# Performance work log

Measured on AMD Instinct MI355X. Metric: run time of the kernel, lower is better.

Reference implementation:

```python
import jax, jax.numpy as jnp
import numpy as np

N = 50000      # nodes
E = 800000     # edges
D = 128        # feature dim
L = 3          # gcn layers
EPS = 1e-5     # batchnorm eps


def setup_inputs() -> dict:
    key = jax.random.key(0)
    ks = jax.random.split(key, 6)
    s = (2.0 / (D + D)) ** 0.5  # xavier-uniform scale proxy
    x = jax.random.normal(ks[0], (N, D), jnp.float32)
    edge_index = jax.random.randint(ks[1], (2, E), 0, N, dtype=jnp.int32)
    conv_w = jax.random.normal(ks[2], (L, D, D), jnp.float32) * s
    conv_b = jnp.zeros((L, D), jnp.float32)
    bn_gamma = jnp.ones((2, D), jnp.float32)
    bn_beta = jnp.zeros((2, D), jnp.float32)
    mlp_w = jax.random.normal(ks[3], (2, D, D), jnp.float32) * s
    mlp_b = jnp.zeros((2, D), jnp.float32)
    out_w = jax.random.normal(ks[4], (D, 1), jnp.float32) * s
    out_b = jnp.zeros((1,), jnp.float32)
    return dict(x=x, edge_index=edge_index, conv_w=conv_w, conv_b=conv_b,
                bn_gamma=bn_gamma, bn_beta=bn_beta, mlp_w=mlp_w, mlp_b=mlp_b,
                out_w=out_w, out_b=out_b)


def _batchnorm(h, gamma, beta):
    # train-mode BN: batch stats over nodes (biased variance, as torch uses for normalization)
    mean = jnp.mean(h, axis=0)
    var = jnp.mean((h - mean) ** 2, axis=0)
    return (h - mean) * jax.lax.rsqrt(var + EPS) * gamma + beta


def reference(x, conv_w, conv_b, bn_gamma, bn_beta, mlp_w, mlp_b, out_w, out_b, edge_index):
    # --- GCN normalization (PyG GCNConv default: add self-loops, sym norm) ---
    loops = jnp.arange(N, dtype=edge_index.dtype)
    src = jnp.concatenate([edge_index[0], loops])  # [E+N]
    dst = jnp.concatenate([edge_index[1], loops])
    deg = jax.ops.segment_sum(jnp.ones_like(dst, jnp.float32), dst, num_segments=N)
    dis = jnp.where(deg > 0, jax.lax.rsqrt(jnp.maximum(deg, 1.0)), 0.0)  # deg^-1/2
    norm = (dis[src] * dis[dst])[:, None]  # [E+N, 1]

    def gcn_conv(h, W, b):
        h = h @ W                                     # [N, D] transform
        msg = h[src] * norm                           # gather + scale, [E+N, D]
        return jax.ops.segment_sum(msg, dst, num_segments=N) + b

    # dropout is identity (training=False)
    h = x
    # layers 0..L-2: conv -> bn -> relu
    for layer in range(L - 1):
        h = gcn_conv(h, conv_w[layer], conv_b[layer])
        h = _batchnorm(h, bn_gamma[layer], bn_beta[layer])
        h = jax.nn.relu(h)
    # last conv: relu(conv), then bns[-1] applied AGAIN (faithful to original quirk)
    h = jax.nn.relu(gcn_conv(h, conv_w[L - 1], conv_b[L - 1]))
    h = _batchnorm(h, bn_gamma[-1], bn_beta[-1])

    # --- MLP classifier head: relu hidden layers, sigmoid output ---
    for i in range(mlp_w.shape[0]):
        h = jax.nn.relu(h @ mlp_w[i] + mlp_b[i])
    out = jax.nn.sigmoid(h @ out_w + out_b)  # [N, 1]
    return out
```

## Files before the change

kernel.cpp:

```cpp
#include <hip/hip_runtime.h>
#include <hip/hip_bf16.h>

#define NN 50000
#define EE 800000
#define DD 128
#define OVCAP 8192

typedef __attribute__((ext_vector_type(8))) short short8;
typedef __attribute__((ext_vector_type(4))) float floatx4;

__device__ __forceinline__ unsigned short f2bf(float f) {
    unsigned int x = __float_as_uint(f);
    unsigned int r = x + 0x7fffu + ((x >> 16) & 1u);
    return (unsigned short)(r >> 16);
}
__device__ __forceinline__ float2 bf2x2(unsigned int u) {
    return make_float2(__uint_as_float(u << 16), __uint_as_float(u & 0xffff0000u));
}

__global__ void k_wprep(const float* __restrict__ conv_w, const float* __restrict__ mlp_w,
                        unsigned short* __restrict__ Wf, unsigned int* __restrict__ hsrow,
                        int* __restrict__ cnt, float* __restrict__ stats,
                        int* __restrict__ ovcnt, int* __restrict__ ell) {
    int g = blockIdx.x * 256 + threadIdx.x;
    if (g < 81920) {
        int m = g >> 14;
        int idx = g & 16383;
        int j  = idx & 7;
        int n  = (idx >> 3) & 15;
        int q  = (idx >> 7) & 3;
        int kk = (idx >> 9) & 3;
        int nt = (idx >> 11) & 1;
        int w  = (idx >> 12) & 3;
        int k = kk * 32 + q * 8 + j;
        int c = w * 32 + nt * 16 + n;
        const float* src = (m < 3) ? (conv_w + m * 16384) : (mlp_w + (m - 3) * 16384);
        Wf[g] = f2bf(src[k * 128 + c]);
    } else if (g < 81984) {
        hsrow[g - 81920] = 0u;
    } else if (g < 133184) {
        cnt[g - 81984] = 0;
    } else if (g < 133952) {
        stats[g - 133184] = 0.f;
    } else if (g < 133968) {
        ovcnt[g - 133952] = 0;
    } else if (g < 533968) {
        ((int4*)ell)[g - 133968] = make_int4(NN, NN, NN, NN);
    }
}

__global__ void k_fill(const int* __restrict__ ei, int* __restrict__ cnt,
                       int* __restrict__ ell, int* __restrict__ ovcnt,
                       int2* __restrict__ ov) {
    const int team = blockIdx.x & 7;
    const int lo = team * 6250, hi = lo + 6250;
    const int tIdx = (blockIdx.x >> 3) * 256 + threadIdx.x;
    for (int e = tIdx; e < EE; e += 65536) {
        int d = ei[EE + e];
        if (d >= lo && d < hi) {
            int s = ei[e];
            if ((unsigned)s < (unsigned)NN) {
                int slot = atomicAdd(&cnt[d], 1);
                if (slot < 32) {
                    ell[d * 32 + slot] = s;
                } else {
                    int op = atomicAdd(ovcnt, 1);
                    if (op < OVCAP) ov[op] = make_int2(d, s);
                }
            }
        }
    }
}

#define LSTR 136
template<int PRO>
__global__ __launch_bounds__(256) void k_gemm_conv(const void* __restrict__ INv,
                                                   const unsigned short* __restrict__ Wf,
                                                   const int* __restrict__ cnt,
                                                   const float* __restrict__ cs,
                                                   const float* __restrict__ css,
                                                   const float* __restrict__ gamma,
                                                   const float* __restrict__ beta,
                                                   unsigned short* __restrict__ OUT) {
    __shared__ unsigned short Al[32 * LSTR];
    __shared__ float bnscL[128], bnshL[128];
    const int tid = threadIdx.x;
    const int lane = tid & 63;
    const int w = tid >> 6;
    const int row0 = blockIdx.x * 32;

    if (PRO) {
        if (tid < 128) {
            const float invn = 1.f / (float)NN;
            float mean = cs[tid] * invn;
            float var = css[tid] * invn - mean * mean;
            float sc = gamma[tid] * rsqrtf(fmaxf(var, 0.f) + 1e-5f);
            bnscL[tid] = sc;
            bnshL[tid] = beta[tid] - mean * sc;
        }
        __syncthreads();
    }

    short8 bf[2][4];
    {
        const uint4* Wq = (const uint4*)Wf;
#pragma unroll
        for (int nt = 0; nt < 2; ++nt)
#pragma unroll
            for (int kk = 0; kk < 4; ++kk) {
                uint4 u = Wq[((w * 2 + nt) * 4 + kk) * 64 + lane];
                bf[nt][kk] = *(short8*)&u;
            }
    }

    {
        int r = tid >> 3, ko8 = (tid & 7) * 16;
        int gr = row0 + r;
        unsigned short tmp[16];
        if (PRO == 0) {
            const float* IN = (const float*)INv;
#pragma unroll
            for (int i = 0; i < 4; ++i) {
                float4 v = make_float4(0.f, 0.f, 0.f, 0.f);
                if (gr < NN) v = *(const float4*)&IN[(size_t)gr * DD + ko8 + i * 4];
                tmp[i * 4 + 0] = f2bf(v.x); tmp[i * 4 + 1] = f2bf(v.y);
                tmp[i * 4 + 2] = f2bf(v.z); tmp[i * 4 + 3] = f2bf(v.w);
            }
        } else {
            const unsigned int* inu = (const unsigned int*)INv;
#pragma unroll
            for (int i = 0; i < 2; ++i) {
                uint4 u = make_uint4(0u, 0u, 0u, 0u);
                if (gr < NN) u = *(const uint4*)&inu[(size_t)gr * 64 + (ko8 >> 1) + i * 4];
                float2 p0 = bf2x2(u.x), p1 = bf2x2(u.y), p2 = bf2x2(u.z), p3 = bf2x2(u.w);
                float vv[8] = {p0.x, p0.y, p1.x, p1.y, p2.x, p2.y, p3.x, p3.y};
#pragma unroll
                for (int j = 0; j < 8; ++j) {
                    float t2 = fmaf(vv[j], bnscL[ko8 + i * 8 + j], bnshL[ko8 + i * 8 + j]);
                    tmp[i * 8 + j] = f2bf(fmaxf(t2, 0.f));
                }
            }
        }
#pragma unroll
        for (int j = 0; j < 2; ++j)
            *(uint4*)&Al[r * LSTR + ko8 + j * 8] = ((uint4*)tmp)[j];
    }
    __syncthreads();

    const int n = lane & 15, q = lane >> 4;
    floatx4 acc[2][2];
#pragma unroll
    for (int mt = 0; mt < 2; ++mt)
#pragma unroll
        for (int nt = 0; nt < 2; ++nt)
            acc[mt][nt] = (floatx4){0.f, 0.f, 0.f, 0.f};

#pragma unroll
    for (int kk = 0; kk < 4; ++kk) {
        int ko = kk * 32 + q * 8;
#pragma unroll
        for (int mt = 0; mt < 2; ++mt) {
            short8 a = *(const short8*)&Al[(mt * 16 + n) * LSTR + ko];
            acc[mt][0] = __builtin_amdgcn_mfma_f32_16x16x32_bf16(a, bf[0][kk], acc[mt][0], 0, 0, 0);
            acc[mt][1] = __builtin_amdgcn_mfma_f32_16x16x32_bf16(a, bf[1][kk], acc[mt][1], 0, 0, 0);
        }
    }

#pragma unroll
    for (int mt = 0; mt < 2; ++mt) {
#pragma unroll
        for (int reg = 0; reg < 4; ++reg) {
            int r = row0 + mt * 16 + q * 4 + reg;
            if (r < NN) {
                float sc = rsqrtf((float)cnt[r] + 1.0f);
                OUT[(size_t)r * DD + w * 32 + n]      = f2bf(acc[mt][0][reg] * sc);
                OUT[(size_t)r * DD + w * 32 + 16 + n] = f2bf(acc[mt][1][reg] * sc);
            }
        }
    }
}

__global__ __launch_bounds__(256) void k_mlp_head(const unsigned int* __restrict__ INu,
                                                  const unsigned short* __restrict__ Wf4,
                                                  const unsigned short* __restrict__ Wf5,
                                                  const float* __restrict__ b4,
                                                  const float* __restrict__ b5,
                                                  const float* __restrict__ cs,
                                                  const float* __restrict__ css,
                                                  const float* __restrict__ gamma,
                                                  const float* __restrict__ beta,
                                                  const float* __restrict__ ow,
                                                  const float* __restrict__ ob,
                                                  float* __restrict__ out) {
    __shared__ unsigned short Al[32 * LSTR];
    __shared__ float bnscL[128], bnshL[128];
    __shared__ float redH[4][32];
    const int tid = threadIdx.x;
    const int lane = tid & 63;
    const int w = tid >> 6;
    const int row0 = blockIdx.x * 32;
    const int n = lane & 15, q = lane >> 4;

    if (tid < 128) {
        const float invn = 1.f / (float)NN;
        float mean = cs[tid] * invn;
        float var = css[tid] * invn - mean * mean;
        float sc = gamma[tid] * rsqrtf(fmaxf(var, 0.f) + 1e-5f);
        bnscL[tid] = sc;
        bnshL[tid] = beta[tid] - mean * sc;
    }
    __syncthreads();

    {
        int r = tid >> 3, ko8 = (tid & 7) * 16;
        int gr = row0 + r;
        unsigned short tmp[16];
#pragma unroll
        for (int i = 0; i < 2; ++i) {
            uint4 u = make_uint4(0u, 0u, 0u, 0u);
            if (gr < NN) u = *(const uint4*)&INu[(size_t)gr * 64 + (ko8 >> 1) + i * 4];
            float2 p0 = bf2x2(u.x), p1 = bf2x2(u.y), p2 = bf2x2(u.z), p3 = bf2x2(u.w);
            float vv[8] = {p0.x, p0.y, p1.x, p1.y, p2.x, p2.y, p3.x, p3.y};
#pragma unroll
            for (int j = 0; j < 8; ++j) {
                float t2 = fmaf(vv[j], bnscL[ko8 + i * 8 + j], bnshL[ko8 + i * 8 + j]);
                tmp[i * 8 + j] = f2bf(t2);
            }
        }
#pragma unroll
        for (int j = 0; j < 2; ++j)
            *(uint4*)&Al[r * LSTR + ko8 + j * 8] = ((uint4*)tmp)[j];
    }
    __syncthreads();

    floatx4 acc[2][2];
#pragma unroll
    for (int mt = 0; mt < 2; ++mt)
#pragma unroll
        for (int nt = 0; nt < 2; ++nt)
            acc[mt][nt] = (floatx4){0.f, 0.f, 0.f, 0.f};
    {
        const uint4* Wq = (const uint4*)Wf4;
#pragma unroll
        for (int kk = 0; kk < 4; ++kk) {
            uint4 u0 = Wq[((w * 2 + 0) * 4 + kk) * 64 + lane];
            uint4 u1 = Wq[((w * 2 + 1) * 4 + kk) * 64 + lane];
            int ko = kk * 32 + q * 8;
#pragma unroll
            for (int mt = 0; mt < 2; ++mt) {
                short8 a = *(const short8*)&Al[(mt * 16 + n) * LSTR + ko];
                acc[mt][0] = __builtin_amdgcn_mfma_f32_16x16x32_bf16(a, *(short8*)&u0, acc[mt][0], 0, 0, 0);
                acc[mt][1] = __builtin_amdgcn_mfma_f32_16x16x32_bf16(a, *(short8*)&u1, acc[mt][1], 0, 0, 0);
            }
        }
    }
    __syncthreads();

    {
        float b0c = b4[w * 32 + n], b1c = b4[w * 32 + 16 + n];
#pragma unroll
        for (int mt = 0; mt < 2; ++mt) {
#pragma unroll
            for (int reg = 0; reg < 4; ++reg) {
                int r = mt * 16 + q * 4 + reg;
                Al[r * LSTR + w * 32 + n]      = f2bf(fmaxf(acc[mt][0][reg] + b0c, 0.f));
                Al[r * LSTR + w * 32 + 16 + n] = f2bf(fmaxf(acc[mt][1][reg] + b1c, 0.f));
            }
        }
    }
    __syncthreads();

#pragma unroll
    for (int mt = 0; mt < 2; ++mt)
#pragma unroll
        for (int nt = 0; nt < 2; ++nt)
            acc[mt][nt] = (floatx4){0.f, 0.f, 0.f, 0.f};
    {
        const uint4* Wq = (const uint4*)Wf5;
#pragma unroll
        for (int kk = 0; kk < 4; ++kk) {
            uint4 u0 = Wq[((w * 2 + 0) * 4 + kk) * 64 + lane];
            uint4 u1 = Wq[((w * 2 + 1) * 4 + kk) * 64 + lane];
            int ko = kk * 32 + q * 8;
#pragma unroll
            for (int mt = 0; mt < 2; ++mt) {
                short8 a = *(const short8*)&Al[(mt * 16 + n) * LSTR + ko];
                acc[mt][0] = __builtin_amdgcn_mfma_f32_16x16x32_bf16(a, *(short8*)&u0, acc[mt][0], 0, 0, 0);
                acc[mt][1] = __builtin_amdgcn_mfma_f32_16x16x32_bf16(a, *(short8*)&u1, acc[mt][1], 0, 0, 0);
            }
        }
    }
    {
        float b0c = b5[w * 32 + n], b1c = b5[w * 32 + 16 + n];
        float w0c = ow[w * 32 + n], w1c = ow[w * 32 + 16 + n];
#pragma unroll
        for (int mt = 0; mt < 2; ++mt) {
#pragma unroll
            for (int reg = 0; reg < 4; ++reg) {
                float h0 = fmaxf(acc[mt][0][reg] + b0c, 0.f);
                float h1 = fmaxf(acc[mt][1][reg] + b1c, 0.f);
                float p = fmaf(h0, w0c, h1 * w1c);
                p += __shfl_xor(p, 1);
                p += __shfl_xor(p, 2);
                p += __shfl_xor(p, 4);
                p += __shfl_xor(p, 8);
                if (n == 0) redH[w][mt * 16 + q * 4 + reg] = p;
            }
        }
        __syncthreads();
        if (tid < 32) {
            int r = row0 + tid;
            if (r < NN) {
                float z = (redH[0][tid] + redH[1][tid]) + (redH[2][tid] + redH[3][tid]) + ob[0];
                out[r] = 1.f / (1.f + expf(-z));
            }
        }
    }
}
#undef LSTR

template<int RELU>
__global__ __launch_bounds__(256) void k_gather(const int* __restrict__ cnt,
                                                const int* __restrict__ ell,
                                                const int2* __restrict__ ov,
                                                const int* __restrict__ ovcnt,
                                                const uint4* __restrict__ HSq,
                                                const float* __restrict__ bias,
                                                unsigned short* __restrict__ OUT,
                                                float* __restrict__ colsum,
                                                float* __restrict__ colsumsq) {
    const int tid = threadIdx.x;
    const int lane = tid & 63;
    const int wid = tid >> 6;
    const int c = lane & 15;
    const int jj = lane >> 4;
    const int gwave = blockIdx.x * 4 + wid;
    const int oc = min(*ovcnt, OVCAP);

    float4 bia0 = ((const float4*)bias)[2 * c];
    float4 bia1 = ((const float4*)bias)[2 * c + 1];
    float sum[8], sq[8];
#pragma unroll
    for (int t = 0; t < 8; ++t) { sum[t] = 0.f; sq[t] = 0.f; }

    const uint4 z4 = make_uint4(0u, 0u, 0u, 0u);
    const int4 iz = make_int4(NN, NN, NN, NN);

    int r = gwave;
    int d = 0;
    int4 ia = iz, ib = iz;
    if (r < NN) {
        d = cnt[r];
        const int4* e4 = (const int4*)(ell + (size_t)r * 32);
        ia = e4[jj];
        ib = e4[jj + 4];
    }

    while (r < NN) {
        uint4 s0 = z4;
        if (jj == 0) s0 = HSq[(size_t)r * 16 + c];
        const bool pa = (ia.x != NN), pb = (ib.x != NN);
        uint4 va[4] = {z4, z4, z4, z4}, vb[4] = {z4, z4, z4, z4};
        if (pa) {
            va[0] = HSq[(size_t)ia.x * 16 + c];
            va[1] = HSq[(size_t)ia.y * 16 + c];
            va[2] = HSq[(size_t)ia.z * 16 + c];
            va[3] = HSq[(size_t)ia.w * 16 + c];
        }
        if (pb) {
            vb[0] = HSq[(size_t)ib.x * 16 + c];
            vb[1] = HSq[(size_t)ib.y * 16 + c];
            vb[2] = HSq[(size_t)ib.z * 16 + c];
            vb[3] = HSq[(size_t)ib.w * 16 + c];
        }

        const int rcur = r, dcur = d;

        r += 8192;
        if (r < NN) {
            d = cnt[r];
            const int4* e4 = (const int4*)(ell + (size_t)r * 32);
            ia = e4[jj];
            ib = e4[jj + 4];
        } else {
            ia = iz; ib = iz;
        }

        float a[8];
#pragma unroll
        for (int t = 0; t < 8; ++t) a[t] = 0.f;
        if (jj == 0) {
            float2 p0 = bf2x2(s0.x), p1 = bf2x2(s0.y), p2 = bf2x2(s0.z), p3 = bf2x2(s0.w);
            a[0] += p0.x; a[1] += p0.y; a[2] += p1.x; a[3] += p1.y;
            a[4] += p2.x; a[5] += p2.y; a[6] += p3.x; a[7] += p3.y;
        }
        if (pa) {
#pragma unroll
            for (int t = 0; t < 4; ++t) {
                float2 p0 = bf2x2(va[t].x), p1 = bf2x2(va[t].y);
                float2 p2 = bf2x2(va[t].z), p3 = bf2x2(va[t].w);
                a[0] += p0.x; a[1] += p0.y; a[2] += p1.x; a[3] += p1.y;
                a[4] += p2.x; a[5] += p2.y; a[6] += p3.x; a[7] += p3.y;
            }
        }
        if (pb) {
#pragma unroll
            for (int t = 0; t < 4; ++t) {
                float2 p0 = bf2x2(vb[t].x), p1 = bf2x2(vb[t].y);
                float2 p2 = bf2x2(vb[t].z), p3 = bf2x2(vb[t].w);
                a[0] += p0.x; a[1] += p0.y; a[2] += p1.x; a[3] += p1.y;
                a[4] += p2.x; a[5] += p2.y; a[6] += p3.x; a[7] += p3.y;
            }
        }
        if (dcur > 32) {
            for (int t = 0; t < oc; ++t) {
                int2 e = ov[t];
                if (jj == 0 && e.x == rcur) {
                    uint4 v = HSq[(size_t)e.y * 16 + c];
                    float2 p0 = bf2x2(v.x), p1 = bf2x2(v.y), p2 = bf2x2(v.z), p3 = bf2x2(v.w);
                    a[0] += p0.x; a[1] += p0.y; a[2] += p1.x; a[3] += p1.y;
                    a[4] += p2.x; a[5] += p2.y; a[6] += p3.x; a[7] += p3.y;
                }
            }
        }

#pragma unroll
        for (int t = 0; t < 8; ++t) {
            a[t] += __shfl_xor(a[t], 16);
            a[t] += __shfl_xor(a[t], 32);
        }

        if (jj == 0) {
            float dr = rsqrtf((float)dcur + 1.0f);
            float v[8];
            v[0] = fmaf(dr, a[0], bia0.x); v[1] = fmaf(dr, a[1], bia0.y);
            v[2] = fmaf(dr, a[2], bia0.z); v[3] = fmaf(dr, a[3], bia0.w);
            v[4] = fmaf(dr, a[4], bia1.x); v[5] = fmaf(dr, a[5], bia1.y);
            v[6] = fmaf(dr, a[6], bia1.z); v[7] = fmaf(dr, a[7], bia1.w);
            if (RELU) {
#pragma unroll
                for (int t = 0; t < 8; ++t) v[t] = fmaxf(v[t], 0.f);
            }
            unsigned int p[4];
#pragma unroll
            for (int t = 0; t < 4; ++t)
                p[t] = (unsigned int)f2bf(v[2 * t]) | ((unsigned int)f2bf(v[2 * t + 1]) << 16);
            *(uint4*)&OUT[(size_t)rcur * DD + c * 8] = make_uint4(p[0], p[1], p[2], p[3]);
#pragma unroll
            for (int t = 0; t < 8; ++t) { sum[t] += v[t]; sq[t] += v[t] * v[t]; }
        }
    }

    __shared__ float redS[4][16][8];
    __shared__ float redQ[4][16][8];
    if (jj == 0) {
#pragma unroll
        for (int t = 0; t < 8; ++t) { redS[wid][c][t] = sum[t]; redQ[wid][c][t] = sq[t]; }
    }
    __syncthreads();
    if (tid < 128) {
        int ci = tid >> 3, ct = tid & 7;
        float S = (redS[0][ci][ct] + redS[1][ci][ct]) + (redS[2][ci][ct] + redS[3][ci][ct]);
        float Q = (redQ[0][ci][ct] + redQ[1][ci][ct]) + (redQ[2][ci][ct] + redQ[3][ci][ct]);
        atomicAdd(&colsum[tid], S);
        atomicAdd(&colsumsq[tid], Q);
    }
}

extern "C" void kernel_launch(void* const* d_in, const int* in_sizes, int n_in,
                              void* d_out, int out_size, void* d_ws, size_t ws_size,
                              hipStream_t stream) {
    const float* x      = (const float*)d_in[0];
    const int*   ei     = (const int*)d_in[1];
    const float* conv_w = (const float*)d_in[2];
    const float* conv_b = (const float*)d_in[3];
    const float* bn_g   = (const float*)d_in[4];
    const float* bn_b   = (const float*)d_in[5];
    const float* mlp_w  = (const float*)d_in[6];
    const float* mlp_b  = (const float*)d_in[7];
    const float* out_w  = (const float*)d_in[8];
    const float* out_b  = (const float*)d_in[9];
    float* out = (float*)d_out;

    const size_t ND4 = (size_t)NN * DD * 4;
    char* ws = (char*)d_ws;
    size_t off = 0;
    unsigned short* B0 = (unsigned short*)(ws + off); off += ND4 / 2;
    unsigned short* B1b = (unsigned short*)(ws + off); off += ND4 / 2 + 256;
    int*   cnt     = (int*)  (ws + off); off += 204800;
    float* cs3     = (float*)(ws + off); off += 3 * 512;
    float* css3    = (float*)(ws + off); off += 3 * 512;
    int*   ovcnt   = (int*)  (ws + off); off += 64;
    int2*  ov      = (int2*) (ws + off); off += OVCAP * 8;
    unsigned short* Wfb = (unsigned short*)(ws + off); off += 5 * 16384 * 2;
    int*   ell     = (int*)  (ws + off); off += (size_t)NN * 32 * 4;

    const int gemm_grid = (NN + 31) / 32;
    const int gather_grid = 2048;

    k_wprep<<<2086, 256, 0, stream>>>(conv_w, mlp_w, Wfb,
        (unsigned int*)(B1b + (size_t)NN * DD), cnt, cs3, ovcnt, ell);

    k_fill<<<2048, 256, 0, stream>>>(ei, cnt, ell, ovcnt, ov);

    k_gemm_conv<0><<<gemm_grid, 256, 0, stream>>>(x, Wfb, cnt,
        nullptr, nullptr, nullptr, nullptr, B1b);
    k_gather<0><<<gather_grid, 256, 0, stream>>>(cnt, ell, ov, ovcnt, (const uint4*)B1b, conv_b, B0, cs3, css3);

    k_gemm_conv<1><<<gemm_grid, 256, 0, stream>>>(B0, Wfb + 16384, cnt,
        cs3, css3, bn_g, bn_b, B1b);
    k_gather<0><<<gather_grid, 256, 0, stream>>>(cnt, ell, ov, ovcnt, (const uint4*)B1b, conv_b + DD, B0, cs3 + 128, css3 + 128);

    k_gemm_conv<1><<<gemm_grid, 256, 0, stream>>>(B0, Wfb + 2 * 16384, cnt,
        cs3 + 128, css3 + 128, bn_g + DD, bn_b + DD, B1b);
    k_gather<1><<<gather_grid, 256, 0, stream>>>(cnt, ell, ov, ovcnt, (const uint4*)B1b, conv_b + 2 * DD, B0, cs3 + 256, css3 + 256);

    k_mlp_head<<<gemm_grid, 256, 0, stream>>>((const unsigned int*)B0, Wfb + 3 * 16384, Wfb + 4 * 16384,
        mlp_b, mlp_b + DD, cs3 + 256, css3 + 256, bn_g + DD, bn_b + DD, out_w, out_b, out);
}
```

Measured before the change: 369.8 us.

## Fuse GCN layers and MLP head into one persistent kernel with grid barriers

Replaces the seven per-stage launches (three GEMMs, three gathers, the MLP head) with a single persistent kernel of 1024 blocks. The blocks loop over row tiles and nodes and separate the stages with a software grid barrier built on global atomics. This removes launch gaps and tail effects between the dependent stages. In exchange, the barrier needs all 1024 blocks to be resident at once, which the launch bound of 4 blocks per CU is meant to ensure, and it depends on bc and bg having been zeroed. The gather stride also changes from 8192 to 4096 waves.

```diff
diff --git a/kernel.cpp b/kernel.cpp
--- a/kernel.cpp
+++ b/kernel.cpp
@@ -5,6 +5,10 @@
 #define EE 800000
 #define DD 128
 #define OVCAP 8192
+#define LSTR 136
+#define NTILE 1563
+#define MGRID 1024
+#define GS 4096
 
 typedef __attribute__((ext_vector_type(8))) short short8;
 typedef __attribute__((ext_vector_type(4))) float floatx4;
@@ -16,6 +20,22 @@
 }
 __device__ __forceinline__ float2 bf2x2(unsigned int u) {
     return make_float2(__uint_as_float(u << 16), __uint_as_float(u & 0xffff0000u));
+}
+
+__device__ __forceinline__ void gsync(int* bc, int* bg) {
+    __syncthreads();
+    if (threadIdx.x == 0) {
+        int g = __hip_atomic_load(bg, __ATOMIC_RELAXED, __HIP_MEMORY_SCOPE_AGENT);
+        int a = __hip_atomic_fetch_add(bc, 1, __ATOMIC_ACQ_REL, __HIP_MEMORY_SCOPE_AGENT);
+        if (a == MGRID - 1) {
+            __hip_atomic_store(bc, 0, __ATOMIC_RELAXED, __HIP_MEMORY_SCOPE_AGENT);
+            __hip_atomic_fetch_add(bg, 1, __ATOMIC_ACQ_REL, __HIP_MEMORY_SCOPE_AGENT);
+        } else {
+            while (__hip_atomic_load(bg, __ATOMIC_ACQUIRE, __HIP_MEMORY_SCOPE_AGENT) == g)
+                __builtin_amdgcn_s_sleep(2);
+        }
+    }
+    __syncthreads();
 }
 
 __global__ void k_wprep(const float* __restrict__ conv_w, const float* __restrict__ mlp_w,
@@ -72,25 +92,265 @@
     }
 }
 
-#define LSTR 136
-template<int PRO>
-__global__ __launch_bounds__(256) void k_gemm_conv(const void* __restrict__ INv,
-                                                   const unsigned short* __restrict__ Wf,
-                                                   const int* __restrict__ cnt,
-                                                   const float* __restrict__ cs,
-                                                   const float* __restrict__ css,
-                                                   const float* __restrict__ gamma,
-                                                   const float* __restrict__ beta,
-                                                   unsigned short* __restrict__ OUT) {
+__global__ __launch_bounds__(256, 4) void k_mega(
+        const float* __restrict__ xin, const int* __restrict__ cnt,
+        const int* __restrict__ ell, const int2* __restrict__ ov,
+        const int* __restrict__ ovcnt, const unsigned short* __restrict__ Wfb,
+        const float* __restrict__ conv_b, const float* __restrict__ bn_g,
+        const float* __restrict__ bn_b, const float* __restrict__ mlp_b,
+        const float* __restrict__ out_w, const float* __restrict__ out_b,
+        unsigned short* __restrict__ B0, unsigned short* __restrict__ B1b,
+        float* __restrict__ cs3, float* __restrict__ css3,
+        float* __restrict__ out, int* __restrict__ bc, int* __restrict__ bg) {
     __shared__ unsigned short Al[32 * LSTR];
     __shared__ float bnscL[128], bnshL[128];
+    __shared__ float redH[4][32];
+    __shared__ float redS[4][16][8];
+    __shared__ float redQ[4][16][8];
+
     const int tid = threadIdx.x;
     const int lane = tid & 63;
     const int w = tid >> 6;
-    const int row0 = blockIdx.x * 32;
-
-    if (PRO) {
+    const int oc = min(*ovcnt, OVCAP);
+    const uint4* HSq = (const uint4*)B1b;
+
+    for (int L = 0; L < 3; ++L) {
+        {
+            const bool pro = (L > 0);
+            if (pro && tid < 128) {
+                const float* cs = cs3 + (L - 1) * 128;
+                const float* css = css3 + (L - 1) * 128;
+                const float* gamma = bn_g + (L - 1) * DD;
+                const float* beta = bn_b + (L - 1) * DD;
+                const float invn = 1.f / (float)NN;
+                float mean = cs[tid] * invn;
+                float var = css[tid] * invn - mean * mean;
+                float sc = gamma[tid] * rsqrtf(fmaxf(var, 0.f) + 1e-5f);
+                bnscL[tid] = sc;
+                bnshL[tid] = beta[tid] - mean * sc;
+            }
+            __syncthreads();
+
+            short8 bf[2][4];
+            {
+                const uint4* Wq = (const uint4*)(Wfb + (size_t)L * 16384);
+#pragma unroll
+                for (int nt = 0; nt < 2; ++nt)
+#pragma unroll
+                    for (int kk = 0; kk < 4; ++kk) {
+                        uint4 u = Wq[((w * 2 + nt) * 4 + kk) * 64 + lane];
+                        bf[nt][kk] = *(short8*)&u;
+                    }
+            }
+            const int n = lane & 15, q = lane >> 4;
+
+            for (int t = blockIdx.x; t < NTILE; t += MGRID) {
+                const int row0 = t * 32;
+                {
+                    int r = tid >> 3, ko8 = (tid & 7) * 16;
+                    int gr = row0 + r;
+                    unsigned short tmp[16];
+                    if (!pro) {
+#pragma unroll
+                        for (int i = 0; i < 4; ++i) {
+                            float4 v = make_float4(0.f, 0.f, 0.f, 0.f);
+                            if (gr < NN) v = *(const float4*)&xin[(size_t)gr * DD + ko8 + i * 4];
+                            tmp[i * 4 + 0] = f2bf(v.x); tmp[i * 4 + 1] = f2bf(v.y);
+                            tmp[i * 4 + 2] = f2bf(v.z); tmp[i * 4 + 3] = f2bf(v.w);
+                        }
+                    } else {
+                        const unsigned int* inu = (const unsigned int*)B0;
+#pragma unroll
+                        for (int i = 0; i < 2; ++i) {
+                            uint4 u = make_uint4(0u, 0u, 0u, 0u);
+                            if (gr < NN) u = *(const uint4*)&inu[(size_t)gr * 64 + (ko8 >> 1) + i * 4];
+                            float2 p0 = bf2x2(u.x), p1 = bf2x2(u.y), p2 = bf2x2(u.z), p3 = bf2x2(u.w);
+                            float vv[8] = {p0.x, p0.y, p1.x, p1.y, p2.x, p2.y, p3.x, p3.y};
+#pragma unroll
+                            for (int j = 0; j < 8; ++j) {
+                                float t2 = fmaf(vv[j], bnscL[ko8 + i * 8 + j], bnshL[ko8 + i * 8 + j]);
+                                tmp[i * 8 + j] = f2bf(fmaxf(t2, 0.f));
+                            }
+                        }
+                    }
+#pragma unroll
+                    for (int j = 0; j < 2; ++j)
+                        *(uint4*)&Al[r * LSTR + ko8 + j * 8] = ((uint4*)tmp)[j];
+                }
+                __syncthreads();
+
+                floatx4 acc[2][2];
+#pragma unroll
+                for (int mt = 0; mt < 2; ++mt)
+#pragma unroll
+                    for (int nt = 0; nt < 2; ++nt)
+                        acc[mt][nt] = (floatx4){0.f, 0.f, 0.f, 0.f};
+#pragma unroll
+                for (int kk = 0; kk < 4; ++kk) {
+                    int ko = kk * 32 + q * 8;
+#pragma unroll
+                    for (int mt = 0; mt < 2; ++mt) {
+                        short8 a = *(const short8*)&Al[(mt * 16 + n) * LSTR + ko];
+                        acc[mt][0] = __builtin_amdgcn_mfma_f32_16x16x32_bf16(a, bf[0][kk], acc[mt][0], 0, 0, 0);
+                        acc[mt][1] = __builtin_amdgcn_mfma_f32_16x16x32_bf16(a, bf[1][kk], acc[mt][1], 0, 0, 0);
+                    }
+                }
+#pragma unroll
+                for (int mt = 0; mt < 2; ++mt) {
+#pragma unroll
+                    for (int reg = 0; reg < 4; ++reg) {
+                        int r = row0 + mt * 16 + q * 4 + reg;
+                        if (r < NN) {
+                            float sc = rsqrtf((float)cnt[r] + 1.0f);
+                            B1b[(size_t)r * DD + w * 32 + n]      = f2bf(acc[mt][0][reg] * sc);
+                            B1b[(size_t)r * DD + w * 32 + 16 + n] = f2bf(acc[mt][1][reg] * sc);
+                        }
+                    }
+                }
+                __syncthreads();
+            }
+        }
+        gsync(bc, bg);
+
+        {
+            const int c = lane & 15, jj = lane >> 4;
+            const float* bias = conv_b + L * DD;
+            const float4 bia0 = ((const float4*)bias)[2 * c];
+            const float4 bia1 = ((const float4*)bias)[2 * c + 1];
+            const bool relu = (L == 2);
+            const uint4 z4 = make_uint4(0u, 0u, 0u, 0u);
+            const int4 iz = make_int4(NN, NN, NN, NN);
+            float sum[8], sq[8];
+#pragma unroll
+            for (int t = 0; t < 8; ++t) { sum[t] = 0.f; sq[t] = 0.f; }
+
+            int r = blockIdx.x * 4 + w;
+            int d = 0;
+            int4 ia = iz, ib = iz;
+            if (r < NN) {
+                d = cnt[r];
+                const int4* e4 = (const int4*)(ell + (size_t)r * 32);
+                ia = e4[jj];
+                ib = e4[jj + 4];
+            }
+
+            while (r < NN) {
+                uint4 s0 = z4;
+                if (jj == 0) s0 = HSq[(size_t)r * 16 + c];
+                const bool pa = (ia.x != NN), pb = (ib.x != NN);
+                uint4 va[4] = {z4, z4, z4, z4}, vb[4] = {z4, z4, z4, z4};
+                if (pa) {
+                    va[0] = HSq[(size_t)ia.x * 16 + c];
+                    va[1] = HSq[(size_t)ia.y * 16 + c];
+                    va[2] = HSq[(size_t)ia.z * 16 + c];
+                    va[3] = HSq[(size_t)ia.w * 16 + c];
+                }
+                if (pb) {
+                    vb[0] = HSq[(size_t)ib.x * 16 + c];
+                    vb[1] = HSq[(size_t)ib.y * 16 + c];
+                    vb[2] = HSq[(size_t)ib.z * 16 + c];
+                    vb[3] = HSq[(size_t)ib.w * 16 + c];
+                }
+
+                const int rcur = r, dcur = d;
+
+                r += GS;
+                if (r < NN) {
+                    d = cnt[r];
+                    const int4* e4 = (const int4*)(ell + (size_t)r * 32);
+                    ia = e4[jj];
+                    ib = e4[jj + 4];
+                } else {
+                    ia = iz; ib = iz;
+                }
+
+                float a[8];
+#pragma unroll
+                for (int t = 0; t < 8; ++t) a[t] = 0.f;
+                if (jj == 0) {
+                    float2 p0 = bf2x2(s0.x), p1 = bf2x2(s0.y), p2 = bf2x2(s0.z), p3 = bf2x2(s0.w);
+                    a[0] += p0.x; a[1] += p0.y; a[2] += p1.x; a[3] += p1.y;
+                    a[4] += p2.x; a[5] += p2.y; a[6] += p3.x; a[7] += p3.y;
+                }
+                if (pa) {
+#pragma unroll
+                    for (int t = 0; t < 4; ++t) {
+                        float2 p0 = bf2x2(va[t].x), p1 = bf2x2(va[t].y);
+                        float2 p2 = bf2x2(va[t].z), p3 = bf2x2(va[t].w);
+                        a[0] += p0.x; a[1] += p0.y; a[2] += p1.x; a[3] += p1.y;
+                        a[4] += p2.x; a[5] += p2.y; a[6] += p3.x; a[7] += p3.y;
+                    }
+                }
+                if (pb) {
+#pragma unroll
+                    for (int t = 0; t < 4; ++t) {
+                        float2 p0 = bf2x2(vb[t].x), p1 = bf2x2(vb[t].y);
+                        float2 p2 = bf2x2(vb[t].z), p3 = bf2x2(vb[t].w);
+                        a[0] += p0.x; a[1] += p0.y; a[2] += p1.x; a[3] += p1.y;
+                        a[4] += p2.x; a[5] += p2.y; a[6] += p3.x; a[7] += p3.y;
+                    }
+                }
+                if (dcur > 32) {
+                    for (int t = 0; t < oc; ++t) {
+                        int2 e = ov[t];
+                        if (jj == 0 && e.x == rcur) {
+                            uint4 v = HSq[(size_t)e.y * 16 + c];
+                            float2 p0 = bf2x2(v.x), p1 = bf2x2(v.y), p2 = bf2x2(v.z), p3 = bf2x2(v.w);
+                            a[0] += p0.x; a[1] += p0.y; a[2] += p1.x; a[3] += p1.y;
+                            a[4] += p2.x; a[5] += p2.y; a[6] += p3.x; a[7] += p3.y;
+                        }
+                    }
+                }
+
+#pragma unroll
+                for (int t = 0; t < 8; ++t) {
+                    a[t] += __shfl_xor(a[t], 16);
+                    a[t] += __shfl_xor(a[t], 32);
+                }
+
+                if (jj == 0) {
+                    float dr = rsqrtf((float)dcur + 1.0f);
+                    float v[8];
+                    v[0] = fmaf(dr, a[0], bia0.x); v[1] = fmaf(dr, a[1], bia0.y);
+                    v[2] = fmaf(dr, a[2], bia0.z); v[3] = fmaf(dr, a[3], bia0.w);
+                    v[4] = fmaf(dr, a[4], bia1.x); v[5] = fmaf(dr, a[5], bia1.y);
+                    v[6] = fmaf(dr, a[6], bia1.z); v[7] = fmaf(dr, a[7], bia1.w);
+                    if (relu) {
+#pragma unroll
+                        for (int t = 0; t < 8; ++t) v[t] = fmaxf(v[t], 0.f);
+                    }
+                    unsigned int p[4];
+#pragma unroll
+                    for (int t = 0; t < 4; ++t)
+                        p[t] = (unsigned int)f2bf(v[2 * t]) | ((unsigned int)f2bf(v[2 * t + 1]) << 16);
+                    *(uint4*)&B0[(size_t)rcur * DD + c * 8] = make_uint4(p[0], p[1], p[2], p[3]);
+#pragma unroll
+                    for (int t = 0; t < 8; ++t) { sum[t] += v[t]; sq[t] += v[t] * v[t]; }
+                }
+            }
+
+            if (jj == 0) {
+#pragma unroll
+                for (int t = 0; t < 8; ++t) { redS[w][c][t] = sum[t]; redQ[w][c][t] = sq[t]; }
+            }
+            __syncthreads();
+            if (tid < 128) {
+                int ci = tid >> 3, ct = tid & 7;
+                float S = (redS[0][ci][ct] + redS[1][ci][ct]) + (redS[2][ci][ct] + redS[3][ci][ct]);
+                float Q = (redQ[0][ci][ct] + redQ[1][ci][ct]) + (redQ[2][ci][ct] + redQ[3][ci][ct]);
+                atomicAdd(&cs3[L * 128 + tid], S);
+                atomicAdd(&css3[L * 128 + tid], Q);
+            }
+        }
+        gsync(bc, bg);
+    }
+
+    {
         if (tid < 128) {
+            const float* cs = cs3 + 256;
+            const float* css = css3 + 256;
+            const float* gamma = bn_g + DD;
+            const float* beta = bn_b + DD;
             const float invn = 1.f / (float)NN;
             float mean = cs[tid] * invn;
             float var = css[tid] * invn - mean * mean;
@@ -99,371 +359,109 @@
             bnshL[tid] = beta[tid] - mean * sc;
         }
         __syncthreads();
-    }
-
-    short8 bf[2][4];
-    {
-        const uint4* Wq = (const uint4*)Wf;
-#pragma unroll
-        for (int nt = 0; nt < 2; ++nt)
+
+        const int n = lane & 15, q = lane >> 4;
+        const unsigned int* INu = (const unsigned int*)B0;
+        const uint4* Wq4 = (const uint4*)(Wfb + 3 * 16384);
+        const uint4* Wq5 = (const uint4*)(Wfb + 4 * 16384);
+        const float b40 = mlp_b[w * 32 + n], b41 = mlp_b[w * 32 + 16 + n];
+        const float b50 = mlp_b[DD + w * 32 + n], b51 = mlp_b[DD + w * 32 + 16 + n];
+        const float w0c = out_w[w * 32 + n], w1c = out_w[w * 32 + 16 + n];
+
+        for (int t = blockIdx.x; t < NTILE; t += MGRID) {
+            const int row0 = t * 32;
+            {
+                int r = tid >> 3, ko8 = (tid & 7) * 16;
+                int gr = row0 + r;
+                unsigned short tmp[16];
+#pragma unroll
+                for (int i = 0; i < 2; ++i) {
+                    uint4 u = make_uint4(0u, 0u, 0u, 0u);
+                    if (gr < NN) u = *(const uint4*)&INu[(size_t)gr * 64 + (ko8 >> 1) + i * 4];
+                    float2 p0 = bf2x2(u.x), p1 = bf2x2(u.y), p2 = bf2x2(u.z), p3 = bf2x2(u.w);
+                    float vv[8] = {p0.x, p0.y, p1.x, p1.y, p2.x, p2.y, p3.x, p3.y};
+#pragma unroll
+                    for (int j = 0; j < 8; ++j) {
+                        float t2 = fmaf(vv[j], bnscL[ko8 + i * 8 + j], bnshL[ko8 + i * 8 + j]);
+                        tmp[i * 8 + j] = f2bf(t2);
+                    }
+                }
+#pragma unroll
+                for (int j = 0; j < 2; ++j)
+                    *(uint4*)&Al[r * LSTR + ko8 + j * 8] = ((uint4*)tmp)[j];
+            }
+            __syncthreads();
+
+            floatx4 acc[2][2];
+#pragma unroll
+            for (int mt = 0; mt < 2; ++mt)
+#pragma unroll
+                for (int nt = 0; nt < 2; ++nt)
+                    acc[mt][nt] = (floatx4){0.f, 0.f, 0.f, 0.f};
 #pragma unroll
             for (int kk = 0; kk < 4; ++kk) {
-                uint4 u = Wq[((w * 2 + nt) * 4 + kk) * 64 + lane];
-                bf[nt][kk] = *(short8*)&u;
-            }
-    }
-
-    {
-        int r = tid >> 3, ko8 = (tid & 7) * 16;
-        int gr = row0 + r;
-        unsigned short tmp[16];
-        if (PRO == 0) {
-            const float* IN = (const float*)INv;
-#pragma unroll
-            for (int i = 0; i < 4; ++i) {
-                float4 v = make_float4(0.f, 0.f, 0.f, 0.f);
-                if (gr < NN) v = *(const float4*)&IN[(size_t)gr * DD + ko8 + i * 4];
-                tmp[i * 4 + 0] = f2bf(v.x); tmp[i * 4 + 1] = f2bf(v.y);
-                tmp[i * 4 + 2] = f2bf(v.z); tmp[i * 4 + 3] = f2bf(v.w);
-            }
-        } else {
-            const unsigned int* inu = (const unsigned int*)INv;
-#pragma unroll
-            for (int i = 0; i < 2; ++i) {
-                uint4 u = make_uint4(0u, 0u, 0u, 0u);
-                if (gr < NN) u = *(const uint4*)&inu[(size_t)gr * 64 + (ko8 >> 1) + i * 4];
-                float2 p0 = bf2x2(u.x), p1 = bf2x2(u.y), p2 = bf2x2(u.z), p3 = bf2x2(u.w);
-                float vv[8] = {p0.x, p0.y, p1.x, p1.y, p2.x, p2.y, p3.x, p3.y};
-#pragma unroll
-                for (int j = 0; j < 8; ++j) {
-                    float t2 = fmaf(vv[j], bnscL[ko8 + i * 8 + j], bnshL[ko8 + i * 8 + j]);
-                    tmp[i * 8 + j] = f2bf(fmaxf(t2, 0.f));
-                }
-            }
+                uint4 u0 = Wq4[((w * 2 + 0) * 4 + kk) * 64 + lane];
+                uint4 u1 = Wq4[((w * 2 + 1) * 4 + kk) * 64 + lane];
+                int ko = kk * 32 + q * 8;
+#pragma unroll
+                for (int mt = 0; mt < 2; ++mt) {
+                    short8 a = *(const short8*)&Al[(mt * 16 + n) * LSTR + ko];
+                    acc[mt][0] = __builtin_amdgcn_mfma_f32_16x16x32_bf16(a, *(short8*)&u0, acc[mt][0], 0, 0, 0);
+                    acc[mt][1] = __builtin_amdgcn_mfma_f32_16x16x32_bf16(a, *(short8*)&u1, acc[mt][1], 0, 0, 0);
+                }
+            }
+            __syncthreads();
+#pragma unroll
+            for (int mt = 0; mt < 2; ++mt) {
+#pragma unroll
+                for (int reg = 0; reg < 4; ++reg) {
+                    int r = mt * 16 + q * 4 + reg;
+                    Al[r * LSTR + w * 32 + n]      = f2bf(fmaxf(acc[mt][0][reg] + b40, 0.f));
+                    Al[r * LSTR + w * 32 + 16 + n] = f2bf(fmaxf(acc[mt][1][reg] + b41, 0.f));
+                }
+            }
+            __syncthreads();
+#pragma unroll
+            for (int mt = 0; mt < 2; ++mt)
+#pragma unroll
+                for (int nt = 0; nt < 2; ++nt)
+                    acc[mt][nt] = (floatx4){0.f, 0.f, 0.f, 0.f};
+#pragma unroll
+            for (int kk = 0; kk < 4; ++kk) {
+                uint4 u0 = Wq5[((w * 2 + 0) * 4 + kk) * 64 + lane];
+                uint4 u1 = Wq5[((w * 2 + 1) * 4 + kk) * 64 + lane];
+                int ko = kk * 32 + q * 8;
+#pragma unroll
+                for (int mt = 0; mt < 2; ++mt) {
+                    short8 a = *(const short8*)&Al[(mt * 16 + n) * LSTR + ko];
+                    acc[mt][0] = __builtin_amdgcn_mfma_f32_16x16x32_bf16(a, *(short8*)&u0, acc[mt][0], 0, 0, 0);
+                    acc[mt][1] = __builtin_amdgcn_mfma_f32_16x16x32_bf16(a, *(short8*)&u1, acc[mt][1], 0, 0, 0);
+                }
+            }
+#pragma unroll
+            for (int mt = 0; mt < 2; ++mt) {
+#pragma unroll
+                for (int reg = 0; reg < 4; ++reg) {
+                    float h0 = fmaxf(acc[mt][0][reg] + b50, 0.f);
+                    float h1 = fmaxf(acc[mt][1][reg] + b51, 0.f);
+                    float p = fmaf(h0, w0c, h1 * w1c);
+                    p += __shfl_xor(p, 1);
+                    p += __shfl_xor(p, 2);
+                    p += __shfl_xor(p, 4);
+                    p += __shfl_xor(p, 8);
+                    if (n == 0) redH[w][mt * 16 + q * 4 + reg] = p;
+                }
+            }
+            __syncthreads();
+            if (tid < 32) {
+                int r = row0 + tid;
+                if (r < NN) {
+                    float z = (redH[0][tid] + redH[1][tid]) + (redH[2][tid] + redH[3][tid]) + out_b[0];
+                    out[r] = 1.f / (1.f + expf(-z));
+                }
+            }
+            __syncthreads();
         }
-#pragma unroll
-        for (int j = 0; j < 2; ++j)
-            *(uint4*)&Al[r * LSTR + ko8 + j * 8] = ((uint4*)tmp)[j];
-    }
-    __syncthreads();
-
-    const int n = lane & 15, q = lane >> 4;
-    floatx4 acc[2][2];
-#pragma unroll
-    for (int mt = 0; mt < 2; ++mt)
-#pragma unroll
-        for (int nt = 0; nt < 2; ++nt)
-            acc[mt][nt] = (floatx4){0.f, 0.f, 0.f, 0.f};
-
-#pragma unroll
-    for (int kk = 0; kk < 4; ++kk) {
-        int ko = kk * 32 + q * 8;
-#pragma unroll
-        for (int mt = 0; mt < 2; ++mt) {
-            short8 a = *(const short8*)&Al[(mt * 16 + n) * LSTR + ko];
-            acc[mt][0] = __builtin_amdgcn_mfma_f32_16x16x32_bf16(a, bf[0][kk], acc[mt][0], 0, 0, 0);
-            acc[mt][1] = __builtin_amdgcn_mfma_f32_16x16x32_bf16(a, bf[1][kk], acc[mt][1], 0, 0, 0);
-        }
-    }
-
-#pragma unroll
-    for (int mt = 0; mt < 2; ++mt) {
-#pragma unroll
-        for (int reg = 0; reg < 4; ++reg) {
-            int r = row0 + mt * 16 + q * 4 + reg;
-            if (r < NN) {
-                float sc = rsqrtf((float)cnt[r] + 1.0f);
-                OUT[(size_t)r * DD + w * 32 + n]      = f2bf(acc[mt][0][reg] * sc);
-                OUT[(size_t)r * DD + w * 32 + 16 + n] = f2bf(acc[mt][1][reg] * sc);
-            }
-        }
-    }
-}
-
-__global__ __launch_bounds__(256) void k_mlp_head(const unsigned int* __restrict__ INu,
-                                                  const unsigned short* __restrict__ Wf4,
-                                                  const unsigned short* __restrict__ Wf5,
-                                                  const float* __restrict__ b4,
-                                                  const float* __restrict__ b5,
-                                                  const float* __restrict__ cs,
-                                                  const float* __restrict__ css,
-                                                  const float* __restrict__ gamma,
-                                                  const float* __restrict__ beta,
-                                                  const float* __restrict__ ow,
-                                                  const float* __restrict__ ob,
-                                                  float* __restrict__ out) {
-    __shared__ unsigned short Al[32 * LSTR];
-    __shared__ float bnscL[128], bnshL[128];
-    __shared__ float redH[4][32];
-    const int tid = threadIdx.x;
-    const int lane = tid & 63;
-    const int w = tid >> 6;
-    const int row0 = blockIdx.x * 32;
-    const int n = lane & 15, q = lane >> 4;
-
-    if (tid < 128) {
-        const float invn = 1.f / (float)NN;
-        float mean = cs[tid] * invn;
-        float var = css[tid] * invn - mean * mean;
-        float sc = gamma[tid] * rsqrtf(fmaxf(var, 0.f) + 1e-5f);
-        bnscL[tid] = sc;
-        bnshL[tid] = beta[tid] - mean * sc;
-    }
-    __syncthreads();
-
-    {
-        int r = tid >> 3, ko8 = (tid & 7) * 16;
-        int gr = row0 + r;
-        unsigned short tmp[16];
-#pragma unroll
-        for (int i = 0; i < 2; ++i) {
-            uint4 u = make_uint4(0u, 0u, 0u, 0u);
-            if (gr < NN) u = *(const uint4*)&INu[(size_t)gr * 64 + (ko8 >> 1) + i * 4];
-            float2 p0 = bf2x2(u.x), p1 = bf2x2(u.y), p2 = bf2x2(u.z), p3 = bf2x2(u.w);
-            float vv[8] = {p0.x, p0.y, p1.x, p1.y, p2.x, p2.y, p3.x, p3.y};
-#pragma unroll
-            for (int j = 0; j < 8; ++j) {
-                float t2 = fmaf(vv[j], bnscL[ko8 + i * 8 + j], bnshL[ko8 + i * 8 + j]);
-                tmp[i * 8 + j] = f2bf(t2);
-            }
-        }
-#pragma unroll
-        for (int j = 0; j < 2; ++j)
-            *(uint4*)&Al[r * LSTR + ko8 + j * 8] = ((uint4*)tmp)[j];
-    }
-    __syncthreads();
-
-    floatx4 acc[2][2];
-#pragma unroll
-    for (int mt = 0; mt < 2; ++mt)
-#pragma unroll
-        for (int nt = 0; nt < 2; ++nt)
-            acc[mt][nt] = (floatx4){0.f, 0.f, 0.f, 0.f};
-    {
-        const uint4* Wq = (const uint4*)Wf4;
-#pragma unroll
-        for (int kk = 0; kk < 4; ++kk) {
-            uint4 u0 = Wq[((w * 2 + 0) * 4 + kk) * 64 + lane];
-            uint4 u1 = Wq[((w * 2 + 1) * 4 + kk) * 64 + lane];
-            int ko = kk * 32 + q * 8;
-#pragma unroll
-            for (int mt = 0; mt < 2; ++mt) {
-                short8 a = *(const short8*)&Al[(mt * 16 + n) * LSTR + ko];
-                acc[mt][0] = __builtin_amdgcn_mfma_f32_16x16x32_bf16(a, *(short8*)&u0, acc[mt][0], 0, 0, 0);
-                acc[mt][1] = __builtin_amdgcn_mfma_f32_16x16x32_bf16(a, *(short8*)&u1, acc[mt][1], 0, 0, 0);
-            }
-        }
-    }
-    __syncthreads();
-
-    {
-        float b0c = b4[w * 32 + n], b1c = b4[w * 32 + 16 + n];
-#pragma unroll
-        for (int mt = 0; mt < 2; ++mt) {
-#pragma unroll
-            for (int reg = 0; reg < 4; ++reg) {
-                int r = mt * 16 + q * 4 + reg;
-                Al[r * LSTR + w * 32 + n]      = f2bf(fmaxf(acc[mt][0][reg] + b0c, 0.f));
-                Al[r * LSTR + w * 32 + 16 + n] = f2bf(fmaxf(acc[mt][1][reg] + b1c, 0.f));
-            }
-        }
-    }
-    __syncthreads();
-
-#pragma unroll
-    for (int mt = 0; mt < 2; ++mt)
-#pragma unroll
-        for (int nt = 0; nt < 2; ++nt)
-            acc[mt][nt] = (floatx4){0.f, 0.f, 0.f, 0.f};
-    {
-        const uint4* Wq = (const uint4*)Wf5;
-#pragma unroll
-        for (int kk = 0; kk < 4; ++kk) {
-            uint4 u0 = Wq[((w * 2 + 0) * 4 + kk) * 64 + lane];
-            uint4 u1 = Wq[((w * 2 + 1) * 4 + kk) * 64 + lane];
-            int ko = kk * 32 + q * 8;
-#pragma unroll
-            for (int mt = 0; mt < 2; ++mt) {
-                short8 a = *(const short8*)&Al[(mt * 16 + n) * LSTR + ko];
-                acc[mt][0] = __builtin_amdgcn_mfma_f32_16x16x32_bf16(a, *(short8*)&u0, acc[mt][0], 0, 0, 0);
-                acc[mt][1] = __builtin_amdgcn_mfma_f32_16x16x32_bf16(a, *(short8*)&u1, acc[mt][1], 0, 0, 0);
-            }
-        }
-    }
-    {
-        float b0c = b5[w * 32 + n], b1c = b5[w * 32 + 16 + n];
-        float w0c = ow[w * 32 + n], w1c = ow[w * 32 + 16 + n];
-#pragma unroll
-        for (int mt = 0; mt < 2; ++mt) {
-#pragma unroll
-            for (int reg = 0; reg < 4; ++reg) {
-                float h0 = fmaxf(acc[mt][0][reg] + b0c, 0.f);
-                float h1 = fmaxf(acc[mt][1][reg] + b1c, 0.f);
-                float p = fmaf(h0, w0c, h1 * w1c);
-                p += __shfl_xor(p, 1);
-                p += __shfl_xor(p, 2);
-                p += __shfl_xor(p, 4);
-                p += __shfl_xor(p, 8);
-                if (n == 0) redH[w][mt * 16 + q * 4 + reg] = p;
-            }
-        }
-        __syncthreads();
-        if (tid < 32) {
-            int r = row0 + tid;
-            if (r < NN) {
-                float z = (redH[0][tid] + redH[1][tid]) + (redH[2][tid] + redH[3][tid]) + ob[0];
-                out[r] = 1.f / (1.f + expf(-z));
-            }
-        }
-    }
-}
-#undef LSTR
-
-template<int RELU>
-__global__ __launch_bounds__(256) void k_gather(const int* __restrict__ cnt,
-                                                const int* __restrict__ ell,
-                                                const int2* __restrict__ ov,
-                                                const int* __restrict__ ovcnt,
-                                                const uint4* __restrict__ HSq,
-                                                const float* __restrict__ bias,
-                                                unsigned short* __restrict__ OUT,
-                                                float* __restrict__ colsum,
-                                                float* __restrict__ colsumsq) {
-    const int tid = threadIdx.x;
-    const int lane = tid & 63;
-    const int wid = tid >> 6;
-    const int c = lane & 15;
-    const int jj = lane >> 4;
-    const int gwave = blockIdx.x * 4 + wid;
-    const int oc = min(*ovcnt, OVCAP);
-
-    float4 bia0 = ((const float4*)bias)[2 * c];
-    float4 bia1 = ((const float4*)bias)[2 * c + 1];
-    float sum[8], sq[8];
-#pragma unroll
-    for (int t = 0; t < 8; ++t) { sum[t] = 0.f; sq[t] = 0.f; }
-
-    const uint4 z4 = make_uint4(0u, 0u, 0u, 0u);
-    const int4 iz = make_int4(NN, NN, NN, NN);
-
-    int r = gwave;
-    int d = 0;
-    int4 ia = iz, ib = iz;
-    if (r < NN) {
-        d = cnt[r];
-        const int4* e4 = (const int4*)(ell + (size_t)r * 32);
-        ia = e4[jj];
-        ib = e4[jj + 4];
-    }
-
-    while (r < NN) {
-        uint4 s0 = z4;
-        if (jj == 0) s0 = HSq[(size_t)r * 16 + c];
-        const bool pa = (ia.x != NN), pb = (ib.x != NN);
-        uint4 va[4] = {z4, z4, z4, z4}, vb[4] = {z4, z4, z4, z4};
-        if (pa) {
-            va[0] = HSq[(size_t)ia.x * 16 + c];
-            va[1] = HSq[(size_t)ia.y * 16 + c];
-            va[2] = HSq[(size_t)ia.z * 16 + c];
-            va[3] = HSq[(size_t)ia.w * 16 + c];
-        }
-        if (pb) {
-            vb[0] = HSq[(size_t)ib.x * 16 + c];
-            vb[1] = HSq[(size_t)ib.y * 16 + c];
-            vb[2] = HSq[(size_t)ib.z * 16 + c];
-            vb[3] = HSq[(size_t)ib.w * 16 + c];
-        }
-
-        const int rcur = r, dcur = d;
-
-        r += 8192;
-        if (r < NN) {
-            d = cnt[r];
-            const int4* e4 = (const int4*)(ell + (size_t)r * 32);
-            ia = e4[jj];
-            ib = e4[jj + 4];
-        } else {
-            ia = iz; ib = iz;
-        }
-
-        float a[8];
-#pragma unroll
-        for (int t = 0; t < 8; ++t) a[t] = 0.f;
-        if (jj == 0) {
-            float2 p0 = bf2x2(s0.x), p1 = bf2x2(s0.y), p2 = bf2x2(s0.z), p3 = bf2x2(s0.w);
-            a[0] += p0.x; a[1] += p0.y; a[2] += p1.x; a[3] += p1.y;
-            a[4] += p2.x; a[5] += p2.y; a[6] += p3.x; a[7] += p3.y;
-        }
-        if (pa) {
-#pragma unroll
-            for (int t = 0; t < 4; ++t) {
-                float2 p0 = bf2x2(va[t].x), p1 = bf2x2(va[t].y);
-                float2 p2 = bf2x2(va[t].z), p3 = bf2x2(va[t].w);
-                a[0] += p0.x; a[1] += p0.y; a[2] += p1.x; a[3] += p1.y;
-                a[4] += p2.x; a[5] += p2.y; a[6] += p3.x; a[7] += p3.y;
-            }
-        }
-        if (pb) {
-#pragma unroll
-            for (int t = 0; t < 4; ++t) {
-                float2 p0 = bf2x2(vb[t].x), p1 = bf2x2(vb[t].y);
-                float2 p2 = bf2x2(vb[t].z), p3 = bf2x2(vb[t].w);
-                a[0] += p0.x; a[1] += p0.y; a[2] += p1.x; a[3] += p1.y;
-                a[4] += p2.x; a[5] += p2.y; a[6] += p3.x; a[7] += p3.y;
-            }
-        }
-        if (dcur > 32) {
-            for (int t = 0; t < oc; ++t) {
-                int2 e = ov[t];
-                if (jj == 0 && e.x == rcur) {
-                    uint4 v = HSq[(size_t)e.y * 16 + c];
-                    float2 p0 = bf2x2(v.x), p1 = bf2x2(v.y), p2 = bf2x2(v.z), p3 = bf2x2(v.w);
-                    a[0] += p0.x; a[1] += p0.y; a[2] += p1.x; a[3] += p1.y;
-                    a[4] += p2.x; a[5] += p2.y; a[6] += p3.x; a[7] += p3.y;
-                }
-            }
-        }
-
-#pragma unroll
-        for (int t = 0; t < 8; ++t) {
-            a[t] += __shfl_xor(a[t], 16);
-            a[t] += __shfl_xor(a[t], 32);
-        }
-
-        if (jj == 0) {
-            float dr = rsqrtf((float)dcur + 1.0f);
-            float v[8];
-            v[0] = fmaf(dr, a[0], bia0.x); v[1] = fmaf(dr, a[1], bia0.y);
-            v[2] = fmaf(dr, a[2], bia0.z); v[3] = fmaf(dr, a[3], bia0.w);
-            v[4] = fmaf(dr, a[4], bia1.x); v[5] = fmaf(dr, a[5], bia1.y);
-            v[6] = fmaf(dr, a[6], bia1.z); v[7] = fmaf(dr, a[7], bia1.w);
-            if (RELU) {
-#pragma unroll
-                for (int t = 0; t < 8; ++t) v[t] = fmaxf(v[t], 0.f);
-            }
-            unsigned int p[4];
-#pragma unroll
-            for (int t = 0; t < 4; ++t)
-                p[t] = (unsigned int)f2bf(v[2 * t]) | ((unsigned int)f2bf(v[2 * t + 1]) << 16);
-            *(uint4*)&OUT[(size_t)rcur * DD + c * 8] = make_uint4(p[0], p[1], p[2], p[3]);
-#pragma unroll
-            for (int t = 0; t < 8; ++t) { sum[t] += v[t]; sq[t] += v[t] * v[t]; }
-        }
-    }
-
-    __shared__ float redS[4][16][8];
-    __shared__ float redQ[4][16][8];
-    if (jj == 0) {
-#pragma unroll
-        for (int t = 0; t < 8; ++t) { redS[wid][c][t] = sum[t]; redQ[wid][c][t] = sq[t]; }
-    }
-    __syncthreads();
-    if (tid < 128) {
-        int ci = tid >> 3, ct = tid & 7;
-        float S = (redS[0][ci][ct] + redS[1][ci][ct]) + (redS[2][ci][ct] + redS[3][ci][ct]);
-        float Q = (redQ[0][ci][ct] + redQ[1][ci][ct]) + (redQ[2][ci][ct] + redQ[3][ci][ct]);
-        atomicAdd(&colsum[tid], S);
-        atomicAdd(&colsumsq[tid], Q);
     }
 }
 
@@ -494,27 +492,14 @@
     int2*  ov      = (int2*) (ws + off); off += OVCAP * 8;
     unsigned short* Wfb = (unsigned short*)(ws + off); off += 5 * 16384 * 2;
     int*   ell     = (int*)  (ws + off); off += (size_t)NN * 32 * 4;
-
-    const int gemm_grid = (NN + 31) / 32;
-    const int gather_grid = 2048;
+    int* bc = ovcnt + 8;
+    int* bg = ovcnt + 9;
 
     k_wprep<<<2086, 256, 0, stream>>>(conv_w, mlp_w, Wfb,
         (unsigned int*)(B1b + (size_t)NN * DD), cnt, cs3, ovcnt, ell);
 
     k_fill<<<2048, 256, 0, stream>>>(ei, cnt, ell, ovcnt, ov);
 
-    k_gemm_conv<0><<<gemm_grid, 256, 0, stream>>>(x, Wfb, cnt,
-        nullptr, nullptr, nullptr, nullptr, B1b);
-    k_gather<0><<<gather_grid, 256, 0, stream>>>(cnt, ell, ov, ovcnt, (const uint4*)B1b, conv_b, B0, cs3, css3);
-
-    k_gemm_conv<1><<<gemm_grid, 256, 0, stream>>>(B0, Wfb + 16384, cnt,
-        cs3, css3, bn_g, bn_b, B1b);
-    k_gather<0><<<gather_grid, 256, 0, stream>>>(cnt, ell, ov, ovcnt, (const uint4*)B1b, conv_b + DD, B0, cs3 + 128, css3 + 128);
-
-    k_gemm_conv<1><<<gemm_grid, 256, 0, stream>>>(B0, Wfb + 2 * 16384, cnt,
-        cs3 + 128, css3 + 128, bn_g + DD, bn_b + DD, B1b);
-    k_gather<1><<<gather_grid, 256, 0, stream>>>(cnt, ell, ov, ovcnt, (const uint4*)B1b, conv_b + 2 * DD, B0, cs3 + 256, css3 + 256);
-
-    k_mlp_head<<<gemm_grid, 256, 0, stream>>>((const unsigned int*)B0, Wfb + 3 * 16384, Wfb + 4 * 16384,
-        mlp_b, mlp_b + DD, cs3 + 256, css3 + 256, bn_g + DD, bn_b + DD, out_w, out_b, out);
-}
+    k_mega<<<MGRID, 256, 0, stream>>>(x, cnt, ell, ov, ovcnt, Wfb,
+        conv_b, bn_g, bn_b, mlp_b, out_w, out_b, B0, B1b, cs3, css3, out, bc, bg);
+}
```

Result: slower. 1.294 ms (+250.0%).
